# Optimization experiments

Measured on AMD Instinct MI355X. Metric: run time of the kernel, lower is better.

Reference implementation:

```python
import jax, jax.numpy as jnp
import numpy as np

SIGMA_S = 1.0
SIGMA_R = 0.1
FR = int(np.ceil(3 * SIGMA_S))          # 3
K_SIZE = 2 * FR + 1                     # 7
B, C, H, W = 8, 3, 512, 512


def matlab_style_gauss2d(shape, sigma):
    m, n = [(ss - 1.0) / 2.0 for ss in shape]
    y, x = np.ogrid[-m:m + 1, -n:n + 1]
    h = np.exp(-(x * x + y * y) / (2.0 * sigma * sigma))
    h[h < np.finfo(h.dtype).eps * h.max()] = 0
    s = h.sum()
    if s != 0:
        h /= s
    return h.astype(np.float32)


GAUSS = matlab_style_gauss2d((K_SIZE, K_SIZE), SIGMA_S)  # [7,7]


def setup_inputs() -> dict:
    key = jax.random.key(0)
    x = jax.random.uniform(key, (B, C, H, W), dtype=jnp.float32)
    return {"input": x}


def reference(input) -> jnp.ndarray:
    # ReflectionPad2d(fr)
    padded = jnp.pad(input, ((0, 0), (0, 0), (FR, FR), (FR, FR)), mode="reflect")
    inv_2sr2 = 1.0 / (2.0 * SIGMA_R * SIGMA_R)
    loss_map = jnp.zeros_like(input)
    for k in range(K_SIZE):
        for l in range(K_SIZE):
            shifted = padded[:, :, k:k + H, l:l + W]            # [B,C,H,W]
            d = input - shifted
            # bilateral range weight * gaussian spatial weight (constant, as in
            # the original which stores weight_map as a raw non-grad tensor)
            w = jax.lax.stop_gradient(
                jnp.exp(-(d * d).sum(1, keepdims=True) * inv_2sr2) * GAUSS[k, l]
            )                                                    # [B,1,H,W]
            loss_map = loss_map + jnp.abs(d) * w
    return loss_map.mean()
```

## Files before the change

### kernel.cpp

```cpp
#include <hip/hip_runtime.h>

#define FR 3
#define KS 7
#define TLX 64
#define TLY 16
#define PPT 2
#define HX (TLX + 2*FR)
#define HY (TLY + FR)
#define LSTR 72
#define IMG_H 512
#define IMG_W 512
#define NB 8
#define NC 3
#define GXB (IMG_W / TLX)
#define GYB (IMG_H / TLY)
#define NMAIN (GXB * GYB * NB)
#define RIM_PER_IMG 6108
#define NRIM_THREADS (RIM_PER_IMG * NB)
#define NRIM_BLK ((NRIM_THREADS + 255) / 256)
#define NBLK_A (NMAIN + NRIM_BLK)
#define NPART NBLK_A

#define KSC 8.493218f
#define K2F 72.134752f

typedef float v2f __attribute__((ext_vector_type(2)));
__device__ __forceinline__ v2f mk2(float a, float b) { v2f r; r.x = a; r.y = b; return r; }

constexpr double g1d[KS] = {0.011108996538242306, 0.1353352832366127,
                            0.6065306597126334,   1.0,
                            0.6065306597126334,   0.1353352832366127,
                            0.011108996538242306};
constexpr double SUMG = 1.0 + 2.0 * (0.011108996538242306 + 0.1353352832366127
                                     + 0.6065306597126334);
constexpr double INVN = 1.0 / (SUMG * SUMG);
constexpr double KD   = 8.493218;
constexpr double WPAIR = 2.0 * INVN / KD;

__device__ __forceinline__ int refl(int i, int n) {
    i = (i < 0) ? -i : i;
    return (i >= n) ? (2*n - 2 - i) : i;
}

__global__ __launch_bounds__(256) void blt_fused(const float* __restrict__ in,
                                                 float* __restrict__ partial) {
    __shared__ float sm[NC][HY][LSTR];
    __shared__ float wsum[4];
    const int tid = threadIdx.x;
    float a = 0.0f;

    if (blockIdx.x >= NRIM_BLK) {
        const int bid = blockIdx.x - NRIM_BLK;
        const int b   = bid >> 8;
        const int rem = bid & 255;
        const int by  = (rem >> 3) * TLY;
        const int bx  = (rem & 7) * TLX;
        const int tx  = tid & 31;
        const int ty  = tid >> 5;
        const float* base = in + (size_t)b * NC * IMG_H * IMG_W;

        for (int idx = tid; idx < HY * HX; idx += 256) {
            int ly = idx / HX;
            int lx = idx - ly * HX;
            int gy = refl(by + ly - FR, IMG_H);
            int gx = refl(bx + lx - FR, IMG_W);
            #pragma unroll
            for (int c = 0; c < NC; ++c)
                sm[c][ly][lx] = base[(c * IMG_H + gy) * IMG_W + gx] * KSC;
        }
        __syncthreads();

        const int x0 = bx + 2 * tx;
        v2f glmv[KS];
        #pragma unroll
        for (int l = 0; l < KS; ++l) {
            float m0 = ((unsigned)(x0 + l - FR)     < (unsigned)IMG_W) ? (float)(g1d[l] * WPAIR) : 0.0f;
            float m1 = ((unsigned)(x0 + 1 + l - FR) < (unsigned)IMG_W) ? (float)(g1d[l] * WPAIR) : 0.0f;
            glmv[l] = mk2(m0, m1);
        }

        const int r0 = ty * PPT;
        v2f ccv[PPT][NC];
        v2f acc[PPT];
        #pragma unroll
        for (int i = 0; i < PPT; ++i) acc[i] = mk2(0.0f, 0.0f);

        #pragma unroll
        for (int rr = PPT + FR - 1; rr >= 0; --rr) {
            v2f wp[NC][KS];
            #pragma unroll
            for (int c = 0; c < NC; ++c) {
                v2f p0 = *reinterpret_cast<const v2f*>(&sm[c][r0 + rr][2 * tx + 0]);
                v2f p1 = *reinterpret_cast<const v2f*>(&sm[c][r0 + rr][2 * tx + 2]);
                v2f p2 = *reinterpret_cast<const v2f*>(&sm[c][r0 + rr][2 * tx + 4]);
                v2f p3 = *reinterpret_cast<const v2f*>(&sm[c][r0 + rr][2 * tx + 6]);
                wp[c][0] = p0;
                wp[c][1] = mk2(p0.y, p1.x);
                wp[c][2] = p1;
                wp[c][3] = mk2(p1.y, p2.x);
                wp[c][4] = p2;
                wp[c][5] = mk2(p2.y, p3.x);
                wp[c][6] = p3;
            }
            #pragma unroll
            for (int i = 0; i < PPT; ++i) {
                const int k = rr - i;
                if (k < 0 || k > FR) continue;
                if (k == FR) {
                    ccv[i][0] = wp[0][3];
                    ccv[i][1] = wp[1][3];
                    ccv[i][2] = wp[2][3];
                }
                const int lmax = (k == FR) ? FR : KS;
                const float rw = (by + r0 + rr >= FR) ? (float)g1d[k] : 0.0f;
                v2f t = mk2(0.0f, 0.0f);
                #pragma unroll
                for (int l = 0; l < KS; ++l) {
                    if (l >= lmax) continue;
                    v2f d0 = ccv[i][0] - wp[0][l];
                    v2f d1 = ccv[i][1] - wp[1][l];
                    v2f d2 = ccv[i][2] - wp[2][l];
                    v2f s  = d0 * d0;
                    s = __builtin_elementwise_fma(d1, d1, s);
                    s = __builtin_elementwise_fma(d2, d2, s);
                    v2f e;
                    e.x = __builtin_amdgcn_exp2f(-s.x);
                    e.y = __builtin_amdgcn_exp2f(-s.y);
                    float sax = fabsf(d0.x) + fabsf(d1.x);
                    sax += fabsf(d2.x);
                    float say = fabsf(d0.y) + fabsf(d1.y);
                    say += fabsf(d2.y);
                    t = __builtin_elementwise_fma(mk2(sax, say), e * glmv[l], t);
                }
                acc[i] = __builtin_elementwise_fma(t, mk2(rw, rw), acc[i]);
            }
        }
        v2f av = acc[0] + acc[1];
        a = av.x + av.y;
    } else {
        const int idx = blockIdx.x * 256 + tid;
        if (idx < NRIM_THREADS) {
            const int b = idx / RIM_PER_IMG;
            int r = idx - b * RIM_PER_IMG;
            int y, x;
            if (r < 3 * IMG_W) { y = r >> 9; x = r & (IMG_W - 1); }
            else if (r < 6 * IMG_W) { r -= 3 * IMG_W; y = (IMG_H - 3) + (r >> 9); x = r & (IMG_W - 1); }
            else if (r < 6 * IMG_W + 3 * (IMG_H - 6)) { r -= 6 * IMG_W; y = 3 + r / 3; x = r - 3 * (r / 3); }
            else { r -= 6 * IMG_W + 3 * (IMG_H - 6); y = 3 + r / 3; x = (IMG_W - 3) + (r - 3 * (r / 3)); }

            const float* base = in + (size_t)b * NC * IMG_H * IMG_W;
            const float cc0 = base[(0 * IMG_H + y) * IMG_W + x];
            const float cc1 = base[(1 * IMG_H + y) * IMG_W + x];
            const float cc2 = base[(2 * IMG_H + y) * IMG_W + x];

            #pragma unroll
            for (int k = 0; k < KS; ++k) {
                #pragma unroll
                for (int l = 0; l < KS; ++l) {
                    if (k == FR && l == FR) continue;
                    int qy = y + k - FR, qx = x + l - FR;
                    bool oob = ((unsigned)qy >= (unsigned)IMG_H) | ((unsigned)qx >= (unsigned)IMG_W);
                    if (oob) {
                        int ry = refl(qy, IMG_H), rx = refl(qx, IMG_W);
                        float v0 = base[(0 * IMG_H + ry) * IMG_W + rx];
                        float v1 = base[(1 * IMG_H + ry) * IMG_W + rx];
                        float v2 = base[(2 * IMG_H + ry) * IMG_W + rx];
                        float d0 = cc0 - v0, d1 = cc1 - v1, d2 = cc2 - v2;
                        float s = d0 * d0;
                        s = fmaf(d1, d1, s);
                        s = fmaf(d2, d2, s);
                        float e = __builtin_amdgcn_exp2f(-(K2F * s));
                        float sa = fabsf(d0) + fabsf(d1) + fabsf(d2);
                        a = fmaf(sa, e * (float)(g1d[k] * g1d[l] * INVN), a);
                    }
                }
            }
        }
        __syncthreads();
    }

    #pragma unroll
    for (int off = 32; off > 0; off >>= 1)
        a += __shfl_down(a, off, 64);
    if ((tid & 63) == 0) wsum[tid >> 6] = a;
    __syncthreads();
    if (tid == 0)
        partial[blockIdx.x] = wsum[0] + wsum[1] + wsum[2] + wsum[3];
}

__global__ __launch_bounds__(256) void finalize_kernel(const float* __restrict__ partial,
                                                       float* __restrict__ out) {
    __shared__ float wsum[4];
    const int tid = threadIdx.x;
    float a = 0.0f;
    for (int i = tid; i < NPART; i += 256) a += partial[i];
    #pragma unroll
    for (int off = 32; off > 0; off >>= 1)
        a += __shfl_down(a, off, 64);
    if ((tid & 63) == 0) wsum[tid >> 6] = a;
    __syncthreads();
    if (tid == 0)
        out[0] = (wsum[0] + wsum[1] + wsum[2] + wsum[3]) / (float)(NB * NC * IMG_H * IMG_W);
}

extern "C" void kernel_launch(void* const* d_in, const int* in_sizes, int n_in,
                              void* d_out, int out_size, void* d_ws, size_t ws_size,
                              hipStream_t stream) {
    const float* in = (const float*)d_in[0];
    float* out = (float*)d_out;
    float* ws  = (float*)d_ws;

    blt_fused<<<NBLK_A, 256, 0, stream>>>(in, ws);
    finalize_kernel<<<1, 256, 0, stream>>>(ws, out);
}
```

Before: 91.65 us.

## Process four pixels per thread on taller tiles and move boundary masks into rim pass

```diff
diff --git a/kernel.cpp b/kernel.cpp
--- a/kernel.cpp
+++ b/kernel.cpp
@@ -3,7 +3,7 @@
 #define FR 3
 #define KS 7
 #define TLX 64
-#define TLY 16
+#define TLY 32
 #define PPT 2
 #define HX (TLX + 2*FR)
 #define HY (TLY + FR)
@@ -25,7 +25,11 @@
 #define K2F 72.134752f
 
 typedef float v2f __attribute__((ext_vector_type(2)));
-__device__ __forceinline__ v2f mk2(float a, float b) { v2f r; r.x = a; r.y = b; return r; }
+typedef float v4f __attribute__((ext_vector_type(4)));
+__device__ __forceinline__ v4f mk4(float a, float b, float c, float d) {
+    v4f r; r.x = a; r.y = b; r.z = c; r.w = d; return r;
+}
+__device__ __forceinline__ v4f sp4(float a) { return mk4(a, a, a, a); }
 
 constexpr double g1d[KS] = {0.011108996538242306, 0.1353352832366127,
                             0.6065306597126334,   1.0,
@@ -42,21 +46,21 @@
     return (i >= n) ? (2*n - 2 - i) : i;
 }
 
-__global__ __launch_bounds__(256) void blt_fused(const float* __restrict__ in,
-                                                 float* __restrict__ partial) {
-    __shared__ float sm[NC][HY][LSTR];
+__global__ __launch_bounds__(256, 4) void blt_fused(const float* __restrict__ in,
+                                                    float* __restrict__ partial) {
+    __shared__ __attribute__((aligned(16))) float sm[NC][HY][LSTR];
     __shared__ float wsum[4];
     const int tid = threadIdx.x;
     float a = 0.0f;
 
     if (blockIdx.x >= NRIM_BLK) {
         const int bid = blockIdx.x - NRIM_BLK;
-        const int b   = bid >> 8;
-        const int rem = bid & 255;
+        const int b   = bid >> 7;
+        const int rem = bid & 127;
         const int by  = (rem >> 3) * TLY;
         const int bx  = (rem & 7) * TLX;
-        const int tx  = tid & 31;
-        const int ty  = tid >> 5;
+        const int tx  = tid & 15;
+        const int ty  = tid >> 4;
         const float* base = in + (size_t)b * NC * IMG_H * IMG_W;
 
         for (int idx = tid; idx < HY * HX; idx += 256) {
@@ -70,73 +74,63 @@
         }
         __syncthreads();
 
-        const int x0 = bx + 2 * tx;
-        v2f glmv[KS];
+        const int r0 = ty * PPT;
+        v4f cc[PPT][NC];
+        v4f acc[PPT];
         #pragma unroll
-        for (int l = 0; l < KS; ++l) {
-            float m0 = ((unsigned)(x0 + l - FR)     < (unsigned)IMG_W) ? (float)(g1d[l] * WPAIR) : 0.0f;
-            float m1 = ((unsigned)(x0 + 1 + l - FR) < (unsigned)IMG_W) ? (float)(g1d[l] * WPAIR) : 0.0f;
-            glmv[l] = mk2(m0, m1);
-        }
-
-        const int r0 = ty * PPT;
-        v2f ccv[PPT][NC];
-        v2f acc[PPT];
-        #pragma unroll
-        for (int i = 0; i < PPT; ++i) acc[i] = mk2(0.0f, 0.0f);
+        for (int i = 0; i < PPT; ++i) acc[i] = sp4(0.0f);
 
         #pragma unroll
         for (int rr = PPT + FR - 1; rr >= 0; --rr) {
-            v2f wp[NC][KS];
-            #pragma unroll
-            for (int c = 0; c < NC; ++c) {
-                v2f p0 = *reinterpret_cast<const v2f*>(&sm[c][r0 + rr][2 * tx + 0]);
-                v2f p1 = *reinterpret_cast<const v2f*>(&sm[c][r0 + rr][2 * tx + 2]);
-                v2f p2 = *reinterpret_cast<const v2f*>(&sm[c][r0 + rr][2 * tx + 4]);
-                v2f p3 = *reinterpret_cast<const v2f*>(&sm[c][r0 + rr][2 * tx + 6]);
-                wp[c][0] = p0;
-                wp[c][1] = mk2(p0.y, p1.x);
-                wp[c][2] = p1;
-                wp[c][3] = mk2(p1.y, p2.x);
-                wp[c][4] = p2;
-                wp[c][5] = mk2(p2.y, p3.x);
-                wp[c][6] = p3;
+            float w0[10], w1[10], w2[10];
+            {
+                const float* rp0 = &sm[0][r0 + rr][4 * tx];
+                *(v4f*)&w0[0] = *(const v4f*)rp0;
+                *(v4f*)&w0[4] = *(const v4f*)(rp0 + 4);
+                *(v2f*)&w0[8] = *(const v2f*)(rp0 + 8);
+                const float* rp1 = &sm[1][r0 + rr][4 * tx];
+                *(v4f*)&w1[0] = *(const v4f*)rp1;
+                *(v4f*)&w1[4] = *(const v4f*)(rp1 + 4);
+                *(v2f*)&w1[8] = *(const v2f*)(rp1 + 8);
+                const float* rp2 = &sm[2][r0 + rr][4 * tx];
+                *(v4f*)&w2[0] = *(const v4f*)rp2;
+                *(v4f*)&w2[4] = *(const v4f*)(rp2 + 4);
+                *(v2f*)&w2[8] = *(const v2f*)(rp2 + 8);
             }
             #pragma unroll
             for (int i = 0; i < PPT; ++i) {
                 const int k = rr - i;
                 if (k < 0 || k > FR) continue;
                 if (k == FR) {
-                    ccv[i][0] = wp[0][3];
-                    ccv[i][1] = wp[1][3];
-                    ccv[i][2] = wp[2][3];
+                    cc[i][0] = mk4(w0[3], w0[4], w0[5], w0[6]);
+                    cc[i][1] = mk4(w1[3], w1[4], w1[5], w1[6]);
+                    cc[i][2] = mk4(w2[3], w2[4], w2[5], w2[6]);
                 }
                 const int lmax = (k == FR) ? FR : KS;
-                const float rw = (by + r0 + rr >= FR) ? (float)g1d[k] : 0.0f;
-                v2f t = mk2(0.0f, 0.0f);
+                v4f t = sp4(0.0f);
                 #pragma unroll
                 for (int l = 0; l < KS; ++l) {
                     if (l >= lmax) continue;
-                    v2f d0 = ccv[i][0] - wp[0][l];
-                    v2f d1 = ccv[i][1] - wp[1][l];
-                    v2f d2 = ccv[i][2] - wp[2][l];
-                    v2f s  = d0 * d0;
+                    v4f d0 = cc[i][0] - mk4(w0[l], w0[l+1], w0[l+2], w0[l+3]);
+                    v4f d1 = cc[i][1] - mk4(w1[l], w1[l+1], w1[l+2], w1[l+3]);
+                    v4f d2 = cc[i][2] - mk4(w2[l], w2[l+1], w2[l+2], w2[l+3]);
+                    v4f s  = d0 * d0;
                     s = __builtin_elementwise_fma(d1, d1, s);
                     s = __builtin_elementwise_fma(d2, d2, s);
-                    v2f e;
+                    v4f e;
                     e.x = __builtin_amdgcn_exp2f(-s.x);
                     e.y = __builtin_amdgcn_exp2f(-s.y);
-                    float sax = fabsf(d0.x) + fabsf(d1.x);
-                    sax += fabsf(d2.x);
-                    float say = fabsf(d0.y) + fabsf(d1.y);
-                    say += fabsf(d2.y);
-                    t = __builtin_elementwise_fma(mk2(sax, say), e * glmv[l], t);
+                    e.z = __builtin_amdgcn_exp2f(-s.z);
+                    e.w = __builtin_amdgcn_exp2f(-s.w);
+                    v4f sa = __builtin_elementwise_abs(d0) + __builtin_elementwise_abs(d1);
+                    sa = sa + __builtin_elementwise_abs(d2);
+                    t = __builtin_elementwise_fma(sa, e * (float)(g1d[l] * WPAIR), t);
                 }
-                acc[i] = __builtin_elementwise_fma(t, mk2(rw, rw), acc[i]);
+                acc[i] = __builtin_elementwise_fma(t, sp4((float)g1d[k]), acc[i]);
             }
         }
-        v2f av = acc[0] + acc[1];
-        a = av.x + av.y;
+        v4f av = acc[0] + acc[1];
+        a = (av.x + av.y) + (av.z + av.w);
     } else {
         const int idx = blockIdx.x * 256 + tid;
         if (idx < NRIM_THREADS) {
@@ -171,7 +165,9 @@
                         s = fmaf(d2, d2, s);
                         float e = __builtin_amdgcn_exp2f(-(K2F * s));
                         float sa = fabsf(d0) + fabsf(d1) + fabsf(d2);
-                        a = fmaf(sa, e * (float)(g1d[k] * g1d[l] * INVN), a);
+                        const bool pos = (k > FR) || (k == FR && l > FR);
+                        const float wkl = (float)(g1d[k] * g1d[l] * INVN * (pos ? 1.0 : -1.0));
+                        a = fmaf(sa, e * wkl, a);
                     }
                 }
             }
```

Result: slower. 94.64 us (+3.3%).

## Drop boundary masks in the tile path and correct them with signed rim terms

Applied to the files above, without the earlier changes.

```diff
diff --git a/kernel.cpp b/kernel.cpp
--- a/kernel.cpp
+++ b/kernel.cpp
@@ -42,9 +42,9 @@
     return (i >= n) ? (2*n - 2 - i) : i;
 }
 
-__global__ __launch_bounds__(256) void blt_fused(const float* __restrict__ in,
-                                                 float* __restrict__ partial) {
-    __shared__ float sm[NC][HY][LSTR];
+__global__ __launch_bounds__(256, 8) void blt_fused(const float* __restrict__ in,
+                                                    float* __restrict__ partial) {
+    __shared__ __attribute__((aligned(16))) float sm[NC][HY][LSTR];
     __shared__ float wsum[4];
     const int tid = threadIdx.x;
     float a = 0.0f;
@@ -70,69 +70,61 @@
         }
         __syncthreads();
 
-        const int x0 = bx + 2 * tx;
-        v2f glmv[KS];
-        #pragma unroll
-        for (int l = 0; l < KS; ++l) {
-            float m0 = ((unsigned)(x0 + l - FR)     < (unsigned)IMG_W) ? (float)(g1d[l] * WPAIR) : 0.0f;
-            float m1 = ((unsigned)(x0 + 1 + l - FR) < (unsigned)IMG_W) ? (float)(g1d[l] * WPAIR) : 0.0f;
-            glmv[l] = mk2(m0, m1);
-        }
-
         const int r0 = ty * PPT;
-        v2f ccv[PPT][NC];
+        v2f cc[PPT][NC];
         v2f acc[PPT];
         #pragma unroll
         for (int i = 0; i < PPT; ++i) acc[i] = mk2(0.0f, 0.0f);
 
         #pragma unroll
         for (int rr = PPT + FR - 1; rr >= 0; --rr) {
-            v2f wp[NC][KS];
+            v2f p0[NC], p1[NC], p2[NC], p3[NC];
             #pragma unroll
             for (int c = 0; c < NC; ++c) {
-                v2f p0 = *reinterpret_cast<const v2f*>(&sm[c][r0 + rr][2 * tx + 0]);
-                v2f p1 = *reinterpret_cast<const v2f*>(&sm[c][r0 + rr][2 * tx + 2]);
-                v2f p2 = *reinterpret_cast<const v2f*>(&sm[c][r0 + rr][2 * tx + 4]);
-                v2f p3 = *reinterpret_cast<const v2f*>(&sm[c][r0 + rr][2 * tx + 6]);
-                wp[c][0] = p0;
-                wp[c][1] = mk2(p0.y, p1.x);
-                wp[c][2] = p1;
-                wp[c][3] = mk2(p1.y, p2.x);
-                wp[c][4] = p2;
-                wp[c][5] = mk2(p2.y, p3.x);
-                wp[c][6] = p3;
+                const float* rp = &sm[c][r0 + rr][2 * tx];
+                p0[c] = *reinterpret_cast<const v2f*>(rp + 0);
+                p1[c] = *reinterpret_cast<const v2f*>(rp + 2);
+                p2[c] = *reinterpret_cast<const v2f*>(rp + 4);
+                p3[c] = *reinterpret_cast<const v2f*>(rp + 6);
             }
             #pragma unroll
             for (int i = 0; i < PPT; ++i) {
                 const int k = rr - i;
                 if (k < 0 || k > FR) continue;
                 if (k == FR) {
-                    ccv[i][0] = wp[0][3];
-                    ccv[i][1] = wp[1][3];
-                    ccv[i][2] = wp[2][3];
+                    #pragma unroll
+                    for (int c = 0; c < NC; ++c)
+                        cc[i][c] = mk2(p1[c].y, p2[c].x);
                 }
                 const int lmax = (k == FR) ? FR : KS;
-                const float rw = (by + r0 + rr >= FR) ? (float)g1d[k] : 0.0f;
                 v2f t = mk2(0.0f, 0.0f);
                 #pragma unroll
                 for (int l = 0; l < KS; ++l) {
                     if (l >= lmax) continue;
-                    v2f d0 = ccv[i][0] - wp[0][l];
-                    v2f d1 = ccv[i][1] - wp[1][l];
-                    v2f d2 = ccv[i][2] - wp[2][l];
+                    v2f w0, w1, w2;
+                    switch (l) {
+                        case 0: w0 = p0[0]; w1 = p0[1]; w2 = p0[2]; break;
+                        case 1: w0 = mk2(p0[0].y, p1[0].x); w1 = mk2(p0[1].y, p1[1].x); w2 = mk2(p0[2].y, p1[2].x); break;
+                        case 2: w0 = p1[0]; w1 = p1[1]; w2 = p1[2]; break;
+                        case 3: w0 = mk2(p1[0].y, p2[0].x); w1 = mk2(p1[1].y, p2[1].x); w2 = mk2(p1[2].y, p2[2].x); break;
+                        case 4: w0 = p2[0]; w1 = p2[1]; w2 = p2[2]; break;
+                        case 5: w0 = mk2(p2[0].y, p3[0].x); w1 = mk2(p2[1].y, p3[1].x); w2 = mk2(p2[2].y, p3[2].x); break;
+                        default: w0 = p3[0]; w1 = p3[1]; w2 = p3[2]; break;
+                    }
+                    v2f d0 = cc[i][0] - w0;
+                    v2f d1 = cc[i][1] - w1;
+                    v2f d2 = cc[i][2] - w2;
                     v2f s  = d0 * d0;
                     s = __builtin_elementwise_fma(d1, d1, s);
                     s = __builtin_elementwise_fma(d2, d2, s);
                     v2f e;
                     e.x = __builtin_amdgcn_exp2f(-s.x);
                     e.y = __builtin_amdgcn_exp2f(-s.y);
-                    float sax = fabsf(d0.x) + fabsf(d1.x);
-                    sax += fabsf(d2.x);
-                    float say = fabsf(d0.y) + fabsf(d1.y);
-                    say += fabsf(d2.y);
-                    t = __builtin_elementwise_fma(mk2(sax, say), e * glmv[l], t);
+                    v2f sa = __builtin_elementwise_abs(d0) + __builtin_elementwise_abs(d1);
+                    sa = sa + __builtin_elementwise_abs(d2);
+                    t = __builtin_elementwise_fma(sa, e * (float)(g1d[l] * WPAIR), t);
                 }
-                acc[i] = __builtin_elementwise_fma(t, mk2(rw, rw), acc[i]);
+                acc[i] = __builtin_elementwise_fma(t, mk2((float)g1d[k], (float)g1d[k]), acc[i]);
             }
         }
         v2f av = acc[0] + acc[1];
@@ -171,7 +163,9 @@
                         s = fmaf(d2, d2, s);
                         float e = __builtin_amdgcn_exp2f(-(K2F * s));
                         float sa = fabsf(d0) + fabsf(d1) + fabsf(d2);
-                        a = fmaf(sa, e * (float)(g1d[k] * g1d[l] * INVN), a);
+                        const bool pos = (k > FR) || (k == FR && l > FR);
+                        const float wkl = (float)(g1d[k] * g1d[l] * INVN * (pos ? 1.0 : -1.0));
+                        a = fmaf(sa, e * wkl, a);
                     }
                 }
             }
```

Result: slower. 96.25 us (+5.0%).
